# Performance work log

Hardware: AMD Instinct MI355X
Metric: run time of the kernel (lower is better)

Reference implementation:

```python
import jax, jax.numpy as jnp
import numpy as np

N_NODES, N_EDGES, N_GRAPHS, H = 20000, 160000, 256, 128
EPS = 1e-5


def setup_inputs() -> dict:
    key = jax.random.key(0)
    it = iter(jax.random.split(key, 64))

    def nk():
        return next(it)

    def lin(fan_in, wshape, bshape):
        s = 1.0 / np.sqrt(fan_in)
        W = jax.random.uniform(nk(), wshape, jnp.float32, -s, s)
        b = jax.random.uniform(nk(), bshape, jnp.float32, -s, s)
        return W, b

    def bn_params(shape):
        g = 1.0 + 0.1 * jax.random.normal(nk(), shape, jnp.float32)
        b = 0.1 * jax.random.normal(nk(), shape, jnp.float32)
        m = 0.1 * jax.random.normal(nk(), shape, jnp.float32)
        v = jax.random.uniform(nk(), shape, jnp.float32, 0.5, 1.5)
        return g, b, m, v

    inp = {}
    inp["x"] = jax.random.normal(nk(), (N_NODES, 10), jnp.float32)
    inp["edge_attr"] = jax.random.normal(nk(), (N_EDGES, 3), jnp.float32)
    inp["edge_index"] = jax.random.randint(nk(), (2, N_EDGES), 0, N_NODES)
    inp["batch"] = jnp.sort(jax.random.randint(nk(), (N_NODES,), 0, N_GRAPHS))
    inp["W_node"], inp["b_node"] = lin(10, (10, H), (H,))
    inp["W_edge"], inp["b_edge"] = lin(3, (3, H), (H,))
    # 10 stacked CGConv layers: lin_f / lin_s each map [2H + H] -> H
    inp["Wf"], inp["bf"] = lin(3 * H, (10, 3 * H, H), (10, H))
    inp["Ws"], inp["bs"] = lin(3 * H, (10, 3 * H, H), (10, H))
    inp["bn_g"], inp["bn_b"], inp["bn_m"], inp["bn_v"] = bn_params((10, H))
    inp["W1"], inp["b1"] = lin(3 * H, (3 * H, 2 * H), (2 * H,))
    inp["bn1_g"], inp["bn1_b"], inp["bn1_m"], inp["bn1_v"] = bn_params((2 * H,))
    inp["W2"], inp["b2"] = lin(2 * H, (2 * H, H), (H,))
    inp["bn2_g"], inp["bn2_b"], inp["bn2_m"], inp["bn2_v"] = bn_params((H,))
    inp["W3"], inp["b3"] = lin(H, (H, H // 2), (H // 2,))
    inp["Wv"], inp["bv"] = lin(H // 2, (H // 2, 1), (1,))
    inp["W_en"], inp["b_en"] = lin(H // 2, (H // 2, 1), (1,))
    inp["Wd"], inp["bd"] = lin(H // 2, (H // 2, 1), (1,))
    inp["Wh"], inp["bh"] = lin(H // 2, (H // 2, 1), (1,))
    return inp


def reference(x, edge_attr, edge_index, batch, W_node, b_node, W_edge, b_edge,
              Wf, bf, Ws, bs, bn_g, bn_b, bn_m, bn_v,
              W1, b1, bn1_g, bn1_b, bn1_m, bn1_v,
              W2, b2, bn2_g, bn2_b, bn2_m, bn2_v,
              W3, b3, Wv, bv, W_en, b_en, Wd, bd, Wh, bh):
    h = jax.nn.relu(x @ W_node + b_node)             # [N, H]
    e = jax.nn.relu(edge_attr @ W_edge + b_edge)     # [E, H]
    src, dst = edge_index[0], edge_index[1]          # PyG: messages src -> dst
    n = h.shape[0]
    for i in range(10):  # fixed layer count, structurally distinct weights
        h_in = h
        z = jnp.concatenate([h[dst], h[src], e], axis=1)          # [E, 3H] = [x_i, x_j, e_ij]
        msg = jax.nn.sigmoid(z @ Wf[i] + bf[i]) * jax.nn.softplus(z @ Ws[i] + bs[i])
        h = h_in + jax.ops.segment_sum(msg, dst, num_segments=n)  # CGConv residual + add-aggr
        h = (h - bn_m[i]) * (bn_g[i] / jnp.sqrt(bn_v[i] + EPS)) + bn_b[i]  # BN (eval)
        h = jax.nn.relu(h)  # dropout is identity in eval
        if i % 2 == 1:
            h = h + h_in
    # global mean / max / add pooling over graphs
    s = jax.ops.segment_sum(h, batch, num_segments=N_GRAPHS)                     # [G, H]
    cnt = jax.ops.segment_sum(jnp.ones((n, 1), h.dtype), batch, num_segments=N_GRAPHS)
    mean = s / jnp.maximum(cnt, 1.0)
    mx = jax.ops.segment_max(h, batch, num_segments=N_GRAPHS)
    g = jnp.concatenate([mean, mx, s], axis=1)                                   # [G, 3H]
    g = jax.nn.relu((g @ W1 + b1 - bn1_m) * (bn1_g / jnp.sqrt(bn1_v + EPS)) + bn1_b)
    g = jax.nn.relu((g @ W2 + b2 - bn2_m) * (bn2_g / jnp.sqrt(bn2_v + EPS)) + bn2_b)
    g = jax.nn.relu(g @ W3 + b3)
    return (g @ Wv + bv, g @ W_en + b_en, g @ Wd + bd, g @ Wh + bh)
```

## Files before the change

kernel.cpp:

```cpp
#include <hip/hip_runtime.h>
#include <hip/hip_bf16.h>
#include <math.h>

#define NN 20000
#define NE 160000
#define NG 256
#define EPSV 1e-5f
#define NQB 2500

typedef short bf16x8 __attribute__((ext_vector_type(8)));
typedef unsigned short u16x8 __attribute__((ext_vector_type(8)));
typedef float f32x4 __attribute__((ext_vector_type(4)));

__device__ __forceinline__ unsigned short f2bf(float f){
  unsigned int u = __float_as_uint(f);
  unsigned int r = (u + 0x7fffu + ((u>>16)&1u)) >> 16;
  return (unsigned short)r;
}
__device__ __forceinline__ float bf2f(unsigned short h){
  return __uint_as_float(((unsigned int)h) << 16);
}
__device__ __forceinline__ float fastmsg(float f, float sv){
  float sg = __builtin_amdgcn_rcpf(1.0f + __expf(-f));
  float sp = fmaxf(sv, 0.0f) + __logf(1.0f + __expf(-fabsf(sv)));
  return sg * sp;
}

__global__ __launch_bounds__(256) void k_hist(const int* __restrict__ ei, int* __restrict__ deg){
  int e = blockIdx.x*256 + threadIdx.x;
  if (e < NE) atomicAdd(&deg[ei[NE+e]], 1);
}
__global__ __launch_bounds__(1024) void k_scan(const int* __restrict__ deg,
                                               int* __restrict__ start, int* __restrict__ cur){
  __shared__ int part[1024];
  int t = threadIdx.x;
  int base = t*20;
  int s = 0;
  for (int j=0;j<20;j++){ int i = base+j; if (i<NN) s += deg[i]; }
  part[t] = s; __syncthreads();
  for (int off=1; off<1024; off<<=1){
    int v = (t >= off) ? part[t-off] : 0;
    __syncthreads();
    part[t] += v;
    __syncthreads();
  }
  int run = (t>0) ? part[t-1] : 0;
  for (int j=0;j<20;j++){
    int i = base+j;
    if (i<NN){ start[i] = run; cur[i] = run; run += deg[i]; }
  }
}
__global__ __launch_bounds__(256) void k_scatter(
    const int* __restrict__ ei, const float* __restrict__ eattr,
    int* __restrict__ cur, int2* __restrict__ esd, float* __restrict__ ea_s){
  int e = blockIdx.x*256 + threadIdx.x;
  if (e >= NE) return;
  int d = ei[NE+e];
  int p = atomicAdd(&cur[d], 1);
  esd[p] = make_int2(ei[e], d);
  ea_s[p*3+0] = eattr[e*3+0];
  ea_s[p*3+1] = eattr[e*3+1];
  ea_s[p*3+2] = eattr[e*3+2];
}

__global__ __launch_bounds__(256) void k_pack_w(
    const float* __restrict__ Wf, const float* __restrict__ Ws,
    unsigned short* __restrict__ Wpk_hi, unsigned short* __restrict__ Wpk_md,
    unsigned short* __restrict__ Wpk_lo)
{
  int idx = blockIdx.x*256 + threadIdx.x;
  if (idx >= 122880) return;
  int l = idx & 63, ks = (idx>>6)&3, nt = (idx>>8)&7;
  int m = idx >> 11;
  int blk = m % 3, gL = m / 3;
  int g = gL & 1, L = gL >> 1;
  const float* src = (g ? Ws : Wf) + (size_t)L*384*128;
  size_t off = (size_t)m*16384 + (nt*4+ks)*512 + l*8;
  int col = nt*16 + (l&15), k0 = ks*32 + (l>>4)*8;
  #pragma unroll
  for (int j=0;j<8;j++){
    float w = src[(size_t)(blk*128 + k0 + j)*128 + col];
    unsigned short hi = f2bf(w);
    float r1 = w - bf2f(hi);
    unsigned short md = f2bf(r1);
    float r2 = r1 - bf2f(md);
    Wpk_hi[off+j] = hi;
    Wpk_md[off+j] = md;
    Wpk_lo[off+j] = f2bf(r2);
  }
}

__global__ __launch_bounds__(256) void k_embed_node(
    const float* __restrict__ x, const float* __restrict__ W, const float* __restrict__ b,
    float* __restrict__ h, float* __restrict__ hacc)
{
  int i = blockIdx.x*256 + threadIdx.x;
  if (i >= NN*128) return;
  int n = i >> 7, c = i & 127;
  float acc = b[c];
  const float* xr = x + n*10;
  #pragma unroll
  for (int k=0;k<10;k++) acc = fmaf(xr[k], W[k*128+c], acc);
  acc = fmaxf(acc, 0.0f);
  h[i] = acc; hacc[i] = acc;
}

__global__ __launch_bounds__(512,2) void k_nodeproj_mfma(
    const float* __restrict__ h,
    const unsigned short* __restrict__ Wpk_hi, const unsigned short* __restrict__ Wpk_md,
    const unsigned short* __restrict__ Wpk_lo,
    const float* __restrict__ bfv, const float* __restrict__ bsv,
    float* __restrict__ Pd, float* __restrict__ Ps)
{
  __shared__ unsigned short wsm[32768];
  int bid = blockIdx.x;
  int m_idx = bid / 157, nblk = bid - m_idx*157;
  int mm = (m_idx==0)?0:(m_idx==1)?1:(m_idx==2)?3:4;
  int t = threadIdx.x;
  {
    const unsigned short* s0 = Wpk_hi + (size_t)mm*16384;
    const unsigned short* s1 = Wpk_md + (size_t)mm*16384;
    #pragma unroll
    for (int ii=0; ii<4; ii++){
      int o = (t + ii*512)*8;
      *(u16x8*)(wsm + o)         = *(const u16x8*)(s0 + o);
      *(u16x8*)(wsm + 16384 + o) = *(const u16x8*)(s1 + o);
    }
  }
  __syncthreads();
  int l = t & 63, w = t >> 6;
  int nb = nblk*128 + w*16;
  if (nb + 16 > NN) return;
  const float* hb = h + (size_t)(nb + (l&15))*128 + (l>>4)*8;
  bf16x8 ah[4], am[4], al[4];
  #pragma unroll
  for (int ks=0;ks<4;ks++){
    #pragma unroll
    for (int j=0;j<8;j++){
      float v = hb[ks*32 + j];
      unsigned short x0 = (unsigned short)(__float_as_uint(v) >> 16);
      float r1 = v - bf2f(x0);
      unsigned short x1 = (unsigned short)(__float_as_uint(r1) >> 16);
      float r2 = r1 - bf2f(x1);
      ah[ks][j] = (short)x0; am[ks][j] = (short)x1; al[ks][j] = (short)f2bf(r2);
    }
  }
  const unsigned short* wl = Wpk_lo + (size_t)mm*16384 + l*8;
  float* OUT = (m_idx & 1) ? Ps : Pd;
  int sel = (m_idx >= 2) ? 1 : 0;
  const float* bias = (m_idx==0) ? bfv : (m_idx==2) ? bsv : nullptr;
  int col0 = l & 15, rg = (l>>4)*4;
  #pragma unroll
  for (int nt=0; nt<8; nt++){
    f32x4 c = {0.f,0.f,0.f,0.f};
    #pragma unroll
    for (int ks=0;ks<4;ks++){
      int fo = (nt*4+ks)*512 + l*8;
      bf16x8 bh = *(const bf16x8*)(wsm + fo);
      bf16x8 bm = *(const bf16x8*)(wsm + 16384 + fo);
      bf16x8 bl = *(const bf16x8*)(wl + (nt*4+ks)*512);
      c = __builtin_amdgcn_mfma_f32_16x16x32_bf16(al[ks], bh, c, 0,0,0);
      c = __builtin_amdgcn_mfma_f32_16x16x32_bf16(am[ks], bm, c, 0,0,0);
      c = __builtin_amdgcn_mfma_f32_16x16x32_bf16(ah[ks], bl, c, 0,0,0);
      c = __builtin_amdgcn_mfma_f32_16x16x32_bf16(am[ks], bh, c, 0,0,0);
      c = __builtin_amdgcn_mfma_f32_16x16x32_bf16(ah[ks], bm, c, 0,0,0);
      c = __builtin_amdgcn_mfma_f32_16x16x32_bf16(ah[ks], bh, c, 0,0,0);
    }
    float bb = bias ? bias[nt*16+col0] : 0.0f;
    #pragma unroll
    for (int r=0;r<4;r++)
      OUT[(size_t)(nb+rg+r)*256 + (nt*16+col0)*2 + sel] = c[r] + bb;
  }
}

__global__ __launch_bounds__(256,4) void k_edge_mfma(
    const float* __restrict__ ea_s, const float* __restrict__ W_edge,
    const float* __restrict__ b_edge,
    const unsigned short* __restrict__ Wpk_hi,
    const unsigned short* __restrict__ Wpk_md,
    const int2* __restrict__ esd,
    const float* __restrict__ Pd, const float* __restrict__ Ps,
    float* __restrict__ hacc)
{
  __shared__ float wlds[512];
  __shared__ unsigned short bfr[16384];
  int bid = blockIdx.x;
  int q = bid / NQB, eg = bid - q*NQB;
  int t = threadIdx.x;
  for (int i=t;i<512;i+=256) wlds[i] = (i<384)? W_edge[i] : b_edge[i-384];
  #pragma unroll
  for (int ii=0; ii<8; ii++){
    int idx = t + ii*256;
    int f = idx >> 6;
    int off = (idx & 63) * 8;
    int g = f >> 4, term = (f>>3)&1, ntl = (f>>2)&1, ks = f&3;
    const unsigned short* src = (term ? Wpk_md : Wpk_hi)
        + (size_t)(g?5:2)*16384 + (size_t)((((q*2+ntl)*4+ks)*512) + off);
    *(u16x8*)(bfr + f*512 + off) = *(const u16x8*)src;
  }
  __syncthreads();
  int l = t & 63, w = t >> 6;
  int e0 = eg*64;
  int row_edge = e0 + w*16 + (l&15);
  float a0 = ea_s[row_edge*3+0], a1 = ea_s[row_edge*3+1], a2 = ea_s[row_edge*3+2];
  int cbase = (l>>4)*8;
  bf16x8 ah[4], al[4];
  #pragma unroll
  for (int ks=0;ks<4;ks++){
    #pragma unroll
    for (int j=0;j<8;j++){
      int c = cbase + ks*32 + j;
      float v = fmaf(a0, wlds[c], fmaf(a1, wlds[128+c], fmaf(a2, wlds[256+c], wlds[384+c])));
      v = fmaxf(v, 0.0f);
      unsigned short hi = (unsigned short)(__float_as_uint(v) >> 16);
      ah[ks][j] = (short)hi;
      al[ks][j] = (short)f2bf(v - bf2f(hi));
    }
  }
  f32x4 accf[2], accs[2];
  #pragma unroll
  for (int ntl=0; ntl<2; ntl++){
    f32x4 cf = {0.f,0.f,0.f,0.f}, cs = {0.f,0.f,0.f,0.f};
    #pragma unroll
    for (int ks=0; ks<4; ks++){
      bf16x8 bh = *(const bf16x8*)(bfr + ((0<<4)|(0<<3)|(ntl<<2)|ks)*512 + l*8);
      bf16x8 bm = *(const bf16x8*)(bfr + ((0<<4)|(1<<3)|(ntl<<2)|ks)*512 + l*8);
      cf = __builtin_amdgcn_mfma_f32_16x16x32_bf16(ah[ks], bh, cf, 0,0,0);
      cf = __builtin_amdgcn_mfma_f32_16x16x32_bf16(ah[ks], bm, cf, 0,0,0);
      cf = __builtin_amdgcn_mfma_f32_16x16x32_bf16(al[ks], bh, cf, 0,0,0);
      bf16x8 sh = *(const bf16x8*)(bfr + ((1<<4)|(0<<3)|(ntl<<2)|ks)*512 + l*8);
      bf16x8 sm = *(const bf16x8*)(bfr + ((1<<4)|(1<<3)|(ntl<<2)|ks)*512 + l*8);
      cs = __builtin_amdgcn_mfma_f32_16x16x32_bf16(ah[ks], sh, cs, 0,0,0);
      cs = __builtin_amdgcn_mfma_f32_16x16x32_bf16(ah[ks], sm, cs, 0,0,0);
      cs = __builtin_amdgcn_mfma_f32_16x16x32_bf16(al[ks], sh, cs, 0,0,0);
    }
    accf[ntl] = cf; accs[ntl] = cs;
  }
  int eb = e0 + w*16, col0 = l & 15, rg = (l>>4)*4;
  int cA = (q*2+0)*16 + col0;
  int cB = (q*2+1)*16 + col0;
  int prev_d = -1;
  float m0 = 0.f, m1 = 0.f;
  float2 pd0, pd1;
  #pragma unroll
  for (int r=0;r<4;r++){
    int p = eb + rg + r;
    int2 sd = esd[p];
    int s = sd.x, d = sd.y;
    if (d != prev_d){
      if (prev_d >= 0){
        atomicAdd(hacc + (size_t)prev_d*128 + cA, m0);
        atomicAdd(hacc + (size_t)prev_d*128 + cB, m1);
      }
      prev_d = d;
      pd0 = *(const float2*)(Pd + (size_t)d*256 + cA*2);
      pd1 = *(const float2*)(Pd + (size_t)d*256 + cB*2);
      m0 = 0.f; m1 = 0.f;
    }
    float2 ps0 = *(const float2*)(Ps + (size_t)s*256 + cA*2);
    float2 ps1 = *(const float2*)(Ps + (size_t)s*256 + cB*2);
    m0 += fastmsg(accf[0][r] + pd0.x + ps0.x, accs[0][r] + pd0.y + ps0.y);
    m1 += fastmsg(accf[1][r] + pd1.x + ps1.x, accs[1][r] + pd1.y + ps1.y);
  }
  atomicAdd(hacc + (size_t)prev_d*128 + cA, m0);
  atomicAdd(hacc + (size_t)prev_d*128 + cB, m1);
}

__global__ __launch_bounds__(256) void k_bn(
    const float* __restrict__ hacc, const float* __restrict__ hin,
    const float* __restrict__ gam, const float* __restrict__ bet,
    const float* __restrict__ mu, const float* __restrict__ var,
    float* __restrict__ hout, float* __restrict__ haccout, int addres)
{
  int i = blockIdx.x*256 + threadIdx.x;
  if (i >= NN*128) return;
  int c = i & 127;
  float scale = gam[c]*rsqrtf(var[c]+EPSV);
  float tv = (hacc[i]-mu[c])*scale + bet[c];
  tv = fmaxf(tv, 0.0f);
  if (addres) tv += hin[i];
  hout[i] = tv; haccout[i] = tv;
}

__global__ __launch_bounds__(256) void k_bn_pool(
    const float* __restrict__ hacc, const float* __restrict__ hin,
    const float* __restrict__ gam, const float* __restrict__ bet,
    const float* __restrict__ mu, const float* __restrict__ var,
    const int* __restrict__ batch,
    float* __restrict__ psum, float* __restrict__ pmax, float* __restrict__ pcnt,
    int addres)
{
  int i = blockIdx.x*256 + threadIdx.x;
  if (i >= NN*128) return;
  int n = i >> 7, c = i & 127;
  float scale = gam[c]*rsqrtf(var[c]+EPSV);
  float tv = (hacc[i]-mu[c])*scale + bet[c];
  tv = fmaxf(tv, 0.0f);
  if (addres) tv += hin[i];
  int b = batch[n];
  atomicAdd(&psum[b*128+c], tv);
  atomicMax((unsigned int*)&pmax[b*128+c], __float_as_uint(tv));
  if (c == 0) atomicAdd(&pcnt[b], 1.0f);
}

__global__ __launch_bounds__(256) void k_mlp1(
    const float* __restrict__ psum, const float* __restrict__ pmax, const float* __restrict__ pcnt,
    const float* __restrict__ W1, const float* __restrict__ b1,
    const float* __restrict__ g1g, const float* __restrict__ g1b,
    const float* __restrict__ g1m, const float* __restrict__ g1v,
    float* __restrict__ out)
{
  int i = blockIdx.x*256 + threadIdx.x;
  int g = i >> 8, c = i & 255;
  float inv = 1.0f / fmaxf(pcnt[g], 1.0f);
  float acc = b1[c];
  for (int k=0;k<128;k++) acc = fmaf(psum[g*128+k]*inv, W1[k*256+c], acc);
  for (int k=0;k<128;k++) acc = fmaf(pmax[g*128+k],     W1[(128+k)*256+c], acc);
  for (int k=0;k<128;k++) acc = fmaf(psum[g*128+k],     W1[(256+k)*256+c], acc);
  float scale = g1g[c]*rsqrtf(g1v[c]+EPSV);
  acc = (acc - g1m[c])*scale + g1b[c];
  out[i] = fmaxf(acc, 0.0f);
}

__global__ __launch_bounds__(256) void k_mlp2(
    const float* __restrict__ g1, const float* __restrict__ W2, const float* __restrict__ b2,
    const float* __restrict__ g2g, const float* __restrict__ g2b,
    const float* __restrict__ g2m, const float* __restrict__ g2v,
    float* __restrict__ out)
{
  int i = blockIdx.x*256 + threadIdx.x;
  int g = i >> 7, c = i & 127;
  float acc = b2[c];
  for (int k=0;k<256;k++) acc = fmaf(g1[g*256+k], W2[k*128+c], acc);
  float scale = g2g[c]*rsqrtf(g2v[c]+EPSV);
  acc = (acc - g2m[c])*scale + g2b[c];
  out[i] = fmaxf(acc, 0.0f);
}

__global__ __launch_bounds__(256) void k_mlp3(
    const float* __restrict__ g2, const float* __restrict__ W3, const float* __restrict__ b3,
    float* __restrict__ out)
{
  int i = blockIdx.x*256 + threadIdx.x;
  int g = i >> 6, c = i & 63;
  float acc = b3[c];
  for (int k=0;k<128;k++) acc = fmaf(g2[g*128+k], W3[k*64+c], acc);
  out[i] = fmaxf(acc, 0.0f);
}

__global__ __launch_bounds__(256) void k_heads(
    const float* __restrict__ g3,
    const float* __restrict__ Wv, const float* __restrict__ bv,
    const float* __restrict__ We, const float* __restrict__ be,
    const float* __restrict__ Wd, const float* __restrict__ bd,
    const float* __restrict__ Wh, const float* __restrict__ bh,
    float* __restrict__ out)
{
  int g = blockIdx.x*256 + threadIdx.x;
  if (g >= NG) return;
  float a0=bv[0], a1=be[0], a2=bd[0], a3=bh[0];
  for (int k=0;k<64;k++){
    float xv = g3[g*64+k];
    a0 = fmaf(xv, Wv[k], a0);
    a1 = fmaf(xv, We[k], a1);
    a2 = fmaf(xv, Wd[k], a2);
    a3 = fmaf(xv, Wh[k], a3);
  }
  out[g] = a0; out[NG+g] = a1; out[2*NG+g] = a2; out[3*NG+g] = a3;
}

extern "C" void kernel_launch(void* const* d_in, const int* in_sizes, int n_in,
                              void* d_out, int out_size, void* d_ws, size_t ws_size,
                              hipStream_t stream)
{
  const float* x         = (const float*)d_in[0];
  const float* edge_attr = (const float*)d_in[1];
  const int*   ei        = (const int*)d_in[2];
  const int*   batch     = (const int*)d_in[3];
  const float* W_node    = (const float*)d_in[4];
  const float* b_node    = (const float*)d_in[5];
  const float* W_edge    = (const float*)d_in[6];
  const float* b_edge    = (const float*)d_in[7];
  const float* Wf        = (const float*)d_in[8];
  const float* bf        = (const float*)d_in[9];
  const float* Ws        = (const float*)d_in[10];
  const float* bs        = (const float*)d_in[11];
  const float* bn_g      = (const float*)d_in[12];
  const float* bn_b      = (const float*)d_in[13];
  const float* bn_m      = (const float*)d_in[14];
  const float* bn_v      = (const float*)d_in[15];
  const float* W1        = (const float*)d_in[16];
  const float* b1        = (const float*)d_in[17];
  const float* bn1_g     = (const float*)d_in[18];
  const float* bn1_b     = (const float*)d_in[19];
  const float* bn1_m     = (const float*)d_in[20];
  const float* bn1_v     = (const float*)d_in[21];
  const float* W2        = (const float*)d_in[22];
  const float* b2        = (const float*)d_in[23];
  const float* bn2_g     = (const float*)d_in[24];
  const float* bn2_b     = (const float*)d_in[25];
  const float* bn2_m     = (const float*)d_in[26];
  const float* bn2_v     = (const float*)d_in[27];
  const float* W3        = (const float*)d_in[28];
  const float* b3        = (const float*)d_in[29];
  const float* Wv        = (const float*)d_in[30];
  const float* bv        = (const float*)d_in[31];
  const float* W_en      = (const float*)d_in[32];
  const float* b_en      = (const float*)d_in[33];
  const float* Wd        = (const float*)d_in[34];
  const float* bd        = (const float*)d_in[35];
  const float* Wh        = (const float*)d_in[36];
  const float* bh        = (const float*)d_in[37];

  float* wsf  = (float*)d_ws;
  float* h    = wsf;
  float* hacc = wsf + 2560000;
  float* Pd   = wsf + 5120000;
  float* Ps   = wsf + 10240000;
  unsigned short* Wpk_hi = (unsigned short*)(wsf + 15360000);
  unsigned short* Wpk_md = (unsigned short*)(wsf + 15851520);
  unsigned short* Wpk_lo = (unsigned short*)(wsf + 16343040);
  float* psum = wsf + 16834560;
  float* pmax = psum + 32768;
  float* pcnt = pmax + 32768;
  float* g1   = pcnt + 256;
  float* g2   = g1 + 65536;
  float* g3   = g2 + 32768;
  int*   deg  = (int*)(wsf + 16982272);
  int*   start= deg + 20000;
  int*   cur  = start + 20000;
  int2*  esd  = (int2*)(cur + 20000);
  float* ea_s = (float*)(cur + 20000 + 320000);

  hipMemsetAsync(deg, 0, 20000*sizeof(int), stream);
  k_hist<<<(NE+255)/256, 256, 0, stream>>>(ei, deg);
  k_scan<<<1, 1024, 0, stream>>>(deg, start, cur);
  k_scatter<<<(NE+255)/256, 256, 0, stream>>>(ei, edge_attr, cur, esd, ea_s);

  k_pack_w<<<480, 256, 0, stream>>>(Wf, Ws, Wpk_hi, Wpk_md, Wpk_lo);
  k_embed_node<<<(NN*128+255)/256, 256, 0, stream>>>(x, W_node, b_node, h, hacc);
  hipMemsetAsync(psum, 0, (size_t)(32768+32768+256)*sizeof(float), stream);

  for (int i=0;i<10;i++){
    const unsigned short* WH = Wpk_hi + (size_t)i*6*16384;
    const unsigned short* WM = Wpk_md + (size_t)i*6*16384;
    const unsigned short* WL = Wpk_lo + (size_t)i*6*16384;
    k_nodeproj_mfma<<<628, 512, 0, stream>>>(h, WH, WM, WL,
        bf + i*128, bs + i*128, Pd, Ps);
    k_edge_mfma<<<4*NQB, 256, 0, stream>>>(ea_s, W_edge, b_edge,
        WH, WM, esd, Pd, Ps, hacc);
    if (i < 9)
      k_bn<<<(NN*128+255)/256, 256, 0, stream>>>(hacc, h,
          bn_g + i*128, bn_b + i*128, bn_m + i*128, bn_v + i*128, h, hacc, i&1);
    else
      k_bn_pool<<<(NN*128+255)/256, 256, 0, stream>>>(hacc, h,
          bn_g + i*128, bn_b + i*128, bn_m + i*128, bn_v + i*128,
          batch, psum, pmax, pcnt, i&1);
  }

  k_mlp1<<<(NG*256)/256, 256, 0, stream>>>(psum, pmax, pcnt, W1, b1, bn1_g, bn1_b, bn1_m, bn1_v, g1);
  k_mlp2<<<(NG*128)/256, 256, 0, stream>>>(g1, W2, b2, bn2_g, bn2_b, bn2_m, bn2_v, g2);
  k_mlp3<<<(NG*64)/256, 256, 0, stream>>>(g2, W3, b3, g3);
  k_heads<<<1, 256, 0, stream>>>(g3, Wv, bv, W_en, b_en, Wd, bd, Wh, bh, (float*)d_out);
}
```

Before: 1.302 ms.

## Fuse batch-norm into node projection and loop column quarters inside the edge kernel

The standalone per-layer BN/ReLU/residual kernel is removed. Its work now happens while the next layer's node projection loads its input, using ping-pong h/acc buffers, and one block group writes the normalized features back for the residual and accumulator. The edge kernel now launches one block per 64-edge group and loops over the four column quarters. It computes the edge embedding and loads edge indices once, reloading the weight fragments between quarters with block barriers. This is meant to save a full read/write pass over node features per layer and avoid redundant edge-embedding work. The cost is fewer, longer edge blocks with extra synchronization, and BN math repeated across projection blocks.

```diff
diff --git a/kernel.cpp b/kernel.cpp
--- a/kernel.cpp
+++ b/kernel.cpp
@@ -6,7 +6,6 @@
 #define NE 160000
 #define NG 256
 #define EPSV 1e-5f
-#define NQB 2500
 
 typedef short bf16x8 __attribute__((ext_vector_type(8)));
 typedef unsigned short u16x8 __attribute__((ext_vector_type(8)));
@@ -106,11 +105,15 @@
 }
 
 __global__ __launch_bounds__(512,2) void k_nodeproj_mfma(
-    const float* __restrict__ h,
+    const float* __restrict__ in_acc, const float* __restrict__ in_h,
+    const float* __restrict__ gam, const float* __restrict__ bet,
+    const float* __restrict__ mu, const float* __restrict__ var,
+    int addres, int dobn,
     const unsigned short* __restrict__ Wpk_hi, const unsigned short* __restrict__ Wpk_md,
     const unsigned short* __restrict__ Wpk_lo,
     const float* __restrict__ bfv, const float* __restrict__ bsv,
-    float* __restrict__ Pd, float* __restrict__ Ps)
+    float* __restrict__ Pd, float* __restrict__ Ps,
+    float* __restrict__ out_h, float* __restrict__ out_acc)
 {
   __shared__ unsigned short wsm[32768];
   int bid = blockIdx.x;
@@ -131,18 +134,35 @@
   int l = t & 63, w = t >> 6;
   int nb = nblk*128 + w*16;
   if (nb + 16 > NN) return;
-  const float* hb = h + (size_t)(nb + (l&15))*128 + (l>>4)*8;
+  size_t base = (size_t)(nb + (l&15))*128 + (l>>4)*8;
+  int cbase = (l>>4)*8;
+  int dowrite = dobn && (m_idx == 0);
   bf16x8 ah[4], am[4], al[4];
   #pragma unroll
   for (int ks=0;ks<4;ks++){
+    float4 w0, w1;
     #pragma unroll
     for (int j=0;j<8;j++){
-      float v = hb[ks*32 + j];
+      float v = in_acc[base + ks*32 + j];
+      if (dobn){
+        int c = cbase + ks*32 + j;
+        float scale = gam[c]*rsqrtf(var[c]+EPSV);
+        v = (v - mu[c])*scale + bet[c];
+        v = fmaxf(v, 0.0f);
+        if (addres) v += in_h[base + ks*32 + j];
+      }
       unsigned short x0 = (unsigned short)(__float_as_uint(v) >> 16);
       float r1 = v - bf2f(x0);
       unsigned short x1 = (unsigned short)(__float_as_uint(r1) >> 16);
       float r2 = r1 - bf2f(x1);
       ah[ks][j] = (short)x0; am[ks][j] = (short)x1; al[ks][j] = (short)f2bf(r2);
+      if (j<4){ ((float*)&w0)[j] = v; } else { ((float*)&w1)[j-4] = v; }
+    }
+    if (dowrite){
+      *(float4*)(out_h  + base + ks*32)     = w0;
+      *(float4*)(out_h  + base + ks*32 + 4) = w1;
+      *(float4*)(out_acc+ base + ks*32)     = w0;
+      *(float4*)(out_acc+ base + ks*32 + 4) = w1;
     }
   }
   const unsigned short* wl = Wpk_lo + (size_t)mm*16384 + l*8;
@@ -184,8 +204,7 @@
 {
   __shared__ float wlds[512];
   __shared__ unsigned short bfr[16384];
-  int bid = blockIdx.x;
-  int q = bid / NQB, eg = bid - q*NQB;
+  int eg = blockIdx.x;
   int t = threadIdx.x;
   for (int i=t;i<512;i+=256) wlds[i] = (i<384)? W_edge[i] : b_edge[i-384];
   #pragma unroll
@@ -195,7 +214,7 @@
     int off = (idx & 63) * 8;
     int g = f >> 4, term = (f>>3)&1, ntl = (f>>2)&1, ks = f&3;
     const unsigned short* src = (term ? Wpk_md : Wpk_hi)
-        + (size_t)(g?5:2)*16384 + (size_t)((((q*2+ntl)*4+ks)*512) + off);
+        + (size_t)(g?5:2)*16384 + (size_t)(((ntl*4+ks)*512) + off);
     *(u16x8*)(bfr + f*512 + off) = *(const u16x8*)src;
   }
   __syncthreads();
@@ -217,69 +236,72 @@
       al[ks][j] = (short)f2bf(v - bf2f(hi));
     }
   }
-  f32x4 accf[2], accs[2];
-  #pragma unroll
-  for (int ntl=0; ntl<2; ntl++){
-    f32x4 cf = {0.f,0.f,0.f,0.f}, cs = {0.f,0.f,0.f,0.f};
-    #pragma unroll
-    for (int ks=0; ks<4; ks++){
-      bf16x8 bh = *(const bf16x8*)(bfr + ((0<<4)|(0<<3)|(ntl<<2)|ks)*512 + l*8);
-      bf16x8 bm = *(const bf16x8*)(bfr + ((0<<4)|(1<<3)|(ntl<<2)|ks)*512 + l*8);
-      cf = __builtin_amdgcn_mfma_f32_16x16x32_bf16(ah[ks], bh, cf, 0,0,0);
-      cf = __builtin_amdgcn_mfma_f32_16x16x32_bf16(ah[ks], bm, cf, 0,0,0);
-      cf = __builtin_amdgcn_mfma_f32_16x16x32_bf16(al[ks], bh, cf, 0,0,0);
-      bf16x8 sh = *(const bf16x8*)(bfr + ((1<<4)|(0<<3)|(ntl<<2)|ks)*512 + l*8);
-      bf16x8 sm = *(const bf16x8*)(bfr + ((1<<4)|(1<<3)|(ntl<<2)|ks)*512 + l*8);
-      cs = __builtin_amdgcn_mfma_f32_16x16x32_bf16(ah[ks], sh, cs, 0,0,0);
-      cs = __builtin_amdgcn_mfma_f32_16x16x32_bf16(ah[ks], sm, cs, 0,0,0);
-      cs = __builtin_amdgcn_mfma_f32_16x16x32_bf16(al[ks], sh, cs, 0,0,0);
-    }
-    accf[ntl] = cf; accs[ntl] = cs;
-  }
   int eb = e0 + w*16, col0 = l & 15, rg = (l>>4)*4;
-  int cA = (q*2+0)*16 + col0;
-  int cB = (q*2+1)*16 + col0;
-  int prev_d = -1;
-  float m0 = 0.f, m1 = 0.f;
-  float2 pd0, pd1;
-  #pragma unroll
-  for (int r=0;r<4;r++){
-    int p = eb + rg + r;
-    int2 sd = esd[p];
-    int s = sd.x, d = sd.y;
-    if (d != prev_d){
-      if (prev_d >= 0){
-        atomicAdd(hacc + (size_t)prev_d*128 + cA, m0);
-        atomicAdd(hacc + (size_t)prev_d*128 + cB, m1);
+  int2 sd[4];
+  #pragma unroll
+  for (int r=0;r<4;r++) sd[r] = esd[eb + rg + r];
+
+  for (int q=0; q<4; q++){
+    f32x4 accf[2], accs[2];
+    #pragma unroll
+    for (int ntl=0; ntl<2; ntl++){
+      f32x4 cf = {0.f,0.f,0.f,0.f}, cs = {0.f,0.f,0.f,0.f};
+      #pragma unroll
+      for (int ks=0; ks<4; ks++){
+        bf16x8 bh = *(const bf16x8*)(bfr + ((0<<4)|(0<<3)|(ntl<<2)|ks)*512 + l*8);
+        bf16x8 bm = *(const bf16x8*)(bfr + ((0<<4)|(1<<3)|(ntl<<2)|ks)*512 + l*8);
+        cf = __builtin_amdgcn_mfma_f32_16x16x32_bf16(ah[ks], bh, cf, 0,0,0);
+        cf = __builtin_amdgcn_mfma_f32_16x16x32_bf16(ah[ks], bm, cf, 0,0,0);
+        cf = __builtin_amdgcn_mfma_f32_16x16x32_bf16(al[ks], bh, cf, 0,0,0);
+        bf16x8 sh = *(const bf16x8*)(bfr + ((1<<4)|(0<<3)|(ntl<<2)|ks)*512 + l*8);
+        bf16x8 sm = *(const bf16x8*)(bfr + ((1<<4)|(1<<3)|(ntl<<2)|ks)*512 + l*8);
+        cs = __builtin_amdgcn_mfma_f32_16x16x32_bf16(ah[ks], sh, cs, 0,0,0);
+        cs = __builtin_amdgcn_mfma_f32_16x16x32_bf16(ah[ks], sm, cs, 0,0,0);
+        cs = __builtin_amdgcn_mfma_f32_16x16x32_bf16(al[ks], sh, cs, 0,0,0);
       }
-      prev_d = d;
-      pd0 = *(const float2*)(Pd + (size_t)d*256 + cA*2);
-      pd1 = *(const float2*)(Pd + (size_t)d*256 + cB*2);
-      m0 = 0.f; m1 = 0.f;
-    }
-    float2 ps0 = *(const float2*)(Ps + (size_t)s*256 + cA*2);
-    float2 ps1 = *(const float2*)(Ps + (size_t)s*256 + cB*2);
-    m0 += fastmsg(accf[0][r] + pd0.x + ps0.x, accs[0][r] + pd0.y + ps0.y);
-    m1 += fastmsg(accf[1][r] + pd1.x + ps1.x, accs[1][r] + pd1.y + ps1.y);
-  }
-  atomicAdd(hacc + (size_t)prev_d*128 + cA, m0);
-  atomicAdd(hacc + (size_t)prev_d*128 + cB, m1);
-}
-
-__global__ __launch_bounds__(256) void k_bn(
-    const float* __restrict__ hacc, const float* __restrict__ hin,
-    const float* __restrict__ gam, const float* __restrict__ bet,
-    const float* __restrict__ mu, const float* __restrict__ var,
-    float* __restrict__ hout, float* __restrict__ haccout, int addres)
-{
-  int i = blockIdx.x*256 + threadIdx.x;
-  if (i >= NN*128) return;
-  int c = i & 127;
-  float scale = gam[c]*rsqrtf(var[c]+EPSV);
-  float tv = (hacc[i]-mu[c])*scale + bet[c];
-  tv = fmaxf(tv, 0.0f);
-  if (addres) tv += hin[i];
-  hout[i] = tv; haccout[i] = tv;
+      accf[ntl] = cf; accs[ntl] = cs;
+    }
+    int cA = (q*2+0)*16 + col0;
+    int cB = (q*2+1)*16 + col0;
+    int prev_d = -1;
+    float m0 = 0.f, m1 = 0.f;
+    float2 pd0, pd1;
+    #pragma unroll
+    for (int r=0;r<4;r++){
+      int s = sd[r].x, d = sd[r].y;
+      if (d != prev_d){
+        if (prev_d >= 0){
+          atomicAdd(hacc + (size_t)prev_d*128 + cA, m0);
+          atomicAdd(hacc + (size_t)prev_d*128 + cB, m1);
+        }
+        prev_d = d;
+        pd0 = *(const float2*)(Pd + (size_t)d*256 + cA*2);
+        pd1 = *(const float2*)(Pd + (size_t)d*256 + cB*2);
+        m0 = 0.f; m1 = 0.f;
+      }
+      float2 ps0 = *(const float2*)(Ps + (size_t)s*256 + cA*2);
+      float2 ps1 = *(const float2*)(Ps + (size_t)s*256 + cB*2);
+      m0 += fastmsg(accf[0][r] + pd0.x + ps0.x, accs[0][r] + pd0.y + ps0.y);
+      m1 += fastmsg(accf[1][r] + pd1.x + ps1.x, accs[1][r] + pd1.y + ps1.y);
+    }
+    atomicAdd(hacc + (size_t)prev_d*128 + cA, m0);
+    atomicAdd(hacc + (size_t)prev_d*128 + cB, m1);
+
+    if (q < 3){
+      __syncthreads();
+      #pragma unroll
+      for (int ii=0; ii<8; ii++){
+        int idx = t + ii*256;
+        int f = idx >> 6;
+        int off = (idx & 63) * 8;
+        int g = f >> 4, term = (f>>3)&1, ntl = (f>>2)&1, ks = f&3;
+        const unsigned short* src = (term ? Wpk_md : Wpk_hi)
+            + (size_t)(g?5:2)*16384 + (size_t)(((((q+1)*2+ntl)*4+ks)*512) + off);
+        *(u16x8*)(bfr + f*512 + off) = *(const u16x8*)src;
+      }
+      __syncthreads();
+    }
+  }
 }
 
 __global__ __launch_bounds__(256) void k_bn_pool(
@@ -413,20 +435,22 @@
   const float* bh        = (const float*)d_in[37];
 
   float* wsf  = (float*)d_ws;
-  float* h    = wsf;
-  float* hacc = wsf + 2560000;
-  float* Pd   = wsf + 5120000;
-  float* Ps   = wsf + 10240000;
-  unsigned short* Wpk_hi = (unsigned short*)(wsf + 15360000);
-  unsigned short* Wpk_md = (unsigned short*)(wsf + 15851520);
-  unsigned short* Wpk_lo = (unsigned short*)(wsf + 16343040);
-  float* psum = wsf + 16834560;
+  float* hA   = wsf;
+  float* accA = wsf + 2560000;
+  float* hB   = wsf + 5120000;
+  float* accB = wsf + 7680000;
+  float* Pd   = wsf + 10240000;
+  float* Ps   = wsf + 15360000;
+  unsigned short* Wpk_hi = (unsigned short*)(wsf + 20480000);
+  unsigned short* Wpk_md = (unsigned short*)(wsf + 20971520);
+  unsigned short* Wpk_lo = (unsigned short*)(wsf + 21463040);
+  float* psum = wsf + 21954560;
   float* pmax = psum + 32768;
   float* pcnt = pmax + 32768;
   float* g1   = pcnt + 256;
   float* g2   = g1 + 65536;
   float* g3   = g2 + 32768;
-  int*   deg  = (int*)(wsf + 16982272);
+  int*   deg  = (int*)(wsf + 22102272);
   int*   start= deg + 20000;
   int*   cur  = start + 20000;
   int2*  esd  = (int2*)(cur + 20000);
@@ -438,25 +462,33 @@
   k_scatter<<<(NE+255)/256, 256, 0, stream>>>(ei, edge_attr, cur, esd, ea_s);
 
   k_pack_w<<<480, 256, 0, stream>>>(Wf, Ws, Wpk_hi, Wpk_md, Wpk_lo);
-  k_embed_node<<<(NN*128+255)/256, 256, 0, stream>>>(x, W_node, b_node, h, hacc);
+  k_embed_node<<<(NN*128+255)/256, 256, 0, stream>>>(x, W_node, b_node, hA, accA);
   hipMemsetAsync(psum, 0, (size_t)(32768+32768+256)*sizeof(float), stream);
 
   for (int i=0;i<10;i++){
     const unsigned short* WH = Wpk_hi + (size_t)i*6*16384;
     const unsigned short* WM = Wpk_md + (size_t)i*6*16384;
     const unsigned short* WL = Wpk_lo + (size_t)i*6*16384;
-    k_nodeproj_mfma<<<628, 512, 0, stream>>>(h, WH, WM, WL,
-        bf + i*128, bs + i*128, Pd, Ps);
-    k_edge_mfma<<<4*NQB, 256, 0, stream>>>(ea_s, W_edge, b_edge,
-        WH, WM, esd, Pd, Ps, hacc);
-    if (i < 9)
-      k_bn<<<(NN*128+255)/256, 256, 0, stream>>>(hacc, h,
-          bn_g + i*128, bn_b + i*128, bn_m + i*128, bn_v + i*128, h, hacc, i&1);
-    else
-      k_bn_pool<<<(NN*128+255)/256, 256, 0, stream>>>(hacc, h,
-          bn_g + i*128, bn_b + i*128, bn_m + i*128, bn_v + i*128,
-          batch, psum, pmax, pcnt, i&1);
-  }
+    float* curH   = (i&1) ? hB   : hA;
+    float* curAcc = (i&1) ? accB : accA;
+    float* prvH   = (i&1) ? hA   : hB;
+    float* prvAcc = (i&1) ? accA : accB;
+    if (i == 0){
+      k_nodeproj_mfma<<<628, 512, 0, stream>>>(hA, hA,
+          bn_g, bn_b, bn_m, bn_v, 0, 0,
+          WH, WM, WL, bf + i*128, bs + i*128, Pd, Ps, hA, accA);
+    } else {
+      k_nodeproj_mfma<<<628, 512, 0, stream>>>(prvAcc, prvH,
+          bn_g + (i-1)*128, bn_b + (i-1)*128, bn_m + (i-1)*128, bn_v + (i-1)*128,
+          (i-1)&1, 1,
+          WH, WM, WL, bf + i*128, bs + i*128, Pd, Ps, curH, curAcc);
+    }
+    k_edge_mfma<<<NE/64, 256, 0, stream>>>(ea_s, W_edge, b_edge,
+        WH, WM, esd, Pd, Ps, curAcc);
+  }
+  k_bn_pool<<<(NN*128+255)/256, 256, 0, stream>>>(accB, hB,
+      bn_g + 9*128, bn_b + 9*128, bn_m + 9*128, bn_v + 9*128,
+      batch, psum, pmax, pcnt, 9&1);
 
   k_mlp1<<<(NG*256)/256, 256, 0, stream>>>(psum, pmax, pcnt, W1, b1, bn1_g, bn1_b, bn1_m, bn1_v, g1);
   k_mlp2<<<(NG*128)/256, 256, 0, stream>>>(g1, W2, b2, bn2_g, bn2_b, bn2_m, bn2_v, g2);
```

Measured after the change: 1.654 ms. +27.1%, slower.

## Loop over column quarters inside edge kernel instead of separate blocks

Applied to the files above, without the earlier changes.

The edge kernel previously launched four blocks per 64-edge group, one per 32-column quarter, each recomputing the edge embedding and reloading edge indices. Now one block handles all four quarters in sequence. It computes the edge embedding and loads src/dst once, then reloads the LDS weight tile between quarters with barriers. This removes redundant embedding math and index loads and cuts the block count fourfold, at the cost of less parallelism and serialized weight reloads with syncs inside the block.

```diff
diff --git a/kernel.cpp b/kernel.cpp
--- a/kernel.cpp
+++ b/kernel.cpp
@@ -6,7 +6,6 @@
 #define NE 160000
 #define NG 256
 #define EPSV 1e-5f
-#define NQB 2500
 
 typedef short bf16x8 __attribute__((ext_vector_type(8)));
 typedef unsigned short u16x8 __attribute__((ext_vector_type(8)));
@@ -184,8 +183,7 @@
 {
   __shared__ float wlds[512];
   __shared__ unsigned short bfr[16384];
-  int bid = blockIdx.x;
-  int q = bid / NQB, eg = bid - q*NQB;
+  int eg = blockIdx.x;
   int t = threadIdx.x;
   for (int i=t;i<512;i+=256) wlds[i] = (i<384)? W_edge[i] : b_edge[i-384];
   #pragma unroll
@@ -195,7 +193,7 @@
     int off = (idx & 63) * 8;
     int g = f >> 4, term = (f>>3)&1, ntl = (f>>2)&1, ks = f&3;
     const unsigned short* src = (term ? Wpk_md : Wpk_hi)
-        + (size_t)(g?5:2)*16384 + (size_t)((((q*2+ntl)*4+ks)*512) + off);
+        + (size_t)(g?5:2)*16384 + (size_t)(((ntl*4+ks)*512) + off);
     *(u16x8*)(bfr + f*512 + off) = *(const u16x8*)src;
   }
   __syncthreads();
@@ -217,53 +215,72 @@
       al[ks][j] = (short)f2bf(v - bf2f(hi));
     }
   }
-  f32x4 accf[2], accs[2];
-  #pragma unroll
-  for (int ntl=0; ntl<2; ntl++){
-    f32x4 cf = {0.f,0.f,0.f,0.f}, cs = {0.f,0.f,0.f,0.f};
-    #pragma unroll
-    for (int ks=0; ks<4; ks++){
-      bf16x8 bh = *(const bf16x8*)(bfr + ((0<<4)|(0<<3)|(ntl<<2)|ks)*512 + l*8);
-      bf16x8 bm = *(const bf16x8*)(bfr + ((0<<4)|(1<<3)|(ntl<<2)|ks)*512 + l*8);
-      cf = __builtin_amdgcn_mfma_f32_16x16x32_bf16(ah[ks], bh, cf, 0,0,0);
-      cf = __builtin_amdgcn_mfma_f32_16x16x32_bf16(ah[ks], bm, cf, 0,0,0);
-      cf = __builtin_amdgcn_mfma_f32_16x16x32_bf16(al[ks], bh, cf, 0,0,0);
-      bf16x8 sh = *(const bf16x8*)(bfr + ((1<<4)|(0<<3)|(ntl<<2)|ks)*512 + l*8);
-      bf16x8 sm = *(const bf16x8*)(bfr + ((1<<4)|(1<<3)|(ntl<<2)|ks)*512 + l*8);
-      cs = __builtin_amdgcn_mfma_f32_16x16x32_bf16(ah[ks], sh, cs, 0,0,0);
-      cs = __builtin_amdgcn_mfma_f32_16x16x32_bf16(ah[ks], sm, cs, 0,0,0);
-      cs = __builtin_amdgcn_mfma_f32_16x16x32_bf16(al[ks], sh, cs, 0,0,0);
-    }
-    accf[ntl] = cf; accs[ntl] = cs;
-  }
   int eb = e0 + w*16, col0 = l & 15, rg = (l>>4)*4;
-  int cA = (q*2+0)*16 + col0;
-  int cB = (q*2+1)*16 + col0;
-  int prev_d = -1;
-  float m0 = 0.f, m1 = 0.f;
-  float2 pd0, pd1;
-  #pragma unroll
-  for (int r=0;r<4;r++){
-    int p = eb + rg + r;
-    int2 sd = esd[p];
-    int s = sd.x, d = sd.y;
-    if (d != prev_d){
-      if (prev_d >= 0){
-        atomicAdd(hacc + (size_t)prev_d*128 + cA, m0);
-        atomicAdd(hacc + (size_t)prev_d*128 + cB, m1);
+  int2 sd[4];
+  #pragma unroll
+  for (int r=0;r<4;r++) sd[r] = esd[eb + rg + r];
+
+  for (int q=0; q<4; q++){
+    f32x4 accf[2], accs[2];
+    #pragma unroll
+    for (int ntl=0; ntl<2; ntl++){
+      f32x4 cf = {0.f,0.f,0.f,0.f}, cs = {0.f,0.f,0.f,0.f};
+      #pragma unroll
+      for (int ks=0; ks<4; ks++){
+        bf16x8 bh = *(const bf16x8*)(bfr + ((0<<4)|(0<<3)|(ntl<<2)|ks)*512 + l*8);
+        bf16x8 bm = *(const bf16x8*)(bfr + ((0<<4)|(1<<3)|(ntl<<2)|ks)*512 + l*8);
+        cf = __builtin_amdgcn_mfma_f32_16x16x32_bf16(ah[ks], bh, cf, 0,0,0);
+        cf = __builtin_amdgcn_mfma_f32_16x16x32_bf16(ah[ks], bm, cf, 0,0,0);
+        cf = __builtin_amdgcn_mfma_f32_16x16x32_bf16(al[ks], bh, cf, 0,0,0);
+        bf16x8 sh = *(const bf16x8*)(bfr + ((1<<4)|(0<<3)|(ntl<<2)|ks)*512 + l*8);
+        bf16x8 sm = *(const bf16x8*)(bfr + ((1<<4)|(1<<3)|(ntl<<2)|ks)*512 + l*8);
+        cs = __builtin_amdgcn_mfma_f32_16x16x32_bf16(ah[ks], sh, cs, 0,0,0);
+        cs = __builtin_amdgcn_mfma_f32_16x16x32_bf16(ah[ks], sm, cs, 0,0,0);
+        cs = __builtin_amdgcn_mfma_f32_16x16x32_bf16(al[ks], sh, cs, 0,0,0);
       }
-      prev_d = d;
-      pd0 = *(const float2*)(Pd + (size_t)d*256 + cA*2);
-      pd1 = *(const float2*)(Pd + (size_t)d*256 + cB*2);
-      m0 = 0.f; m1 = 0.f;
-    }
-    float2 ps0 = *(const float2*)(Ps + (size_t)s*256 + cA*2);
-    float2 ps1 = *(const float2*)(Ps + (size_t)s*256 + cB*2);
-    m0 += fastmsg(accf[0][r] + pd0.x + ps0.x, accs[0][r] + pd0.y + ps0.y);
-    m1 += fastmsg(accf[1][r] + pd1.x + ps1.x, accs[1][r] + pd1.y + ps1.y);
-  }
-  atomicAdd(hacc + (size_t)prev_d*128 + cA, m0);
-  atomicAdd(hacc + (size_t)prev_d*128 + cB, m1);
+      accf[ntl] = cf; accs[ntl] = cs;
+    }
+    int cA = (q*2+0)*16 + col0;
+    int cB = (q*2+1)*16 + col0;
+    int prev_d = -1;
+    float m0 = 0.f, m1 = 0.f;
+    float2 pd0, pd1;
+    #pragma unroll
+    for (int r=0;r<4;r++){
+      int s = sd[r].x, d = sd[r].y;
+      if (d != prev_d){
+        if (prev_d >= 0){
+          atomicAdd(hacc + (size_t)prev_d*128 + cA, m0);
+          atomicAdd(hacc + (size_t)prev_d*128 + cB, m1);
+        }
+        prev_d = d;
+        pd0 = *(const float2*)(Pd + (size_t)d*256 + cA*2);
+        pd1 = *(const float2*)(Pd + (size_t)d*256 + cB*2);
+        m0 = 0.f; m1 = 0.f;
+      }
+      float2 ps0 = *(const float2*)(Ps + (size_t)s*256 + cA*2);
+      float2 ps1 = *(const float2*)(Ps + (size_t)s*256 + cB*2);
+      m0 += fastmsg(accf[0][r] + pd0.x + ps0.x, accs[0][r] + pd0.y + ps0.y);
+      m1 += fastmsg(accf[1][r] + pd1.x + ps1.x, accs[1][r] + pd1.y + ps1.y);
+    }
+    atomicAdd(hacc + (size_t)prev_d*128 + cA, m0);
+    atomicAdd(hacc + (size_t)prev_d*128 + cB, m1);
+
+    if (q < 3){
+      __syncthreads();
+      #pragma unroll
+      for (int ii=0; ii<8; ii++){
+        int idx = t + ii*256;
+        int f = idx >> 6;
+        int off = (idx & 63) * 8;
+        int g = f >> 4, term = (f>>3)&1, ntl = (f>>2)&1, ks = f&3;
+        const unsigned short* src = (term ? Wpk_md : Wpk_hi)
+            + (size_t)(g?5:2)*16384 + (size_t)(((((q+1)*2+ntl)*4+ks)*512) + off);
+        *(u16x8*)(bfr + f*512 + off) = *(const u16x8*)src;
+      }
+      __syncthreads();
+    }
+  }
 }
 
 __global__ __launch_bounds__(256) void k_bn(
@@ -447,7 +464,7 @@
     const unsigned short* WL = Wpk_lo + (size_t)i*6*16384;
     k_nodeproj_mfma<<<628, 512, 0, stream>>>(h, WH, WM, WL,
         bf + i*128, bs + i*128, Pd, Ps);
-    k_edge_mfma<<<4*NQB, 256, 0, stream>>>(ea_s, W_edge, b_edge,
+    k_edge_mfma<<<NE/64, 256, 0, stream>>>(ea_s, W_edge, b_edge,
         WH, WM, esd, Pd, Ps, hacc);
     if (i < 9)
       k_bn<<<(NN*128+255)/256, 256, 0, stream>>>(hacc, h,
```

Result: slower. 1.333 ms (+2.4%).
